# Optimization experiments

Hardware: AMD Instinct MI355X
Metric: run time of the kernel (lower is better)

## Reference

```python
import jax, jax.numpy as jnp
import numpy as np

N_NODES = 150000  # n_users + n_items
N_EDGES = 2400000
D = 128
LEAKY_SLOPE = 0.2  # tf.nn.leaky_relu default alpha
L2_EPS = 1e-12     # tf.math.l2_normalize epsilon


def setup_inputs() -> dict:
    key = jax.random.key(0)
    ks = jax.random.split(key, 8)
    edge_row = jax.random.randint(ks[0], (N_EDGES,), 0, N_NODES, dtype=jnp.int32)
    edge_col = jax.random.randint(ks[1], (N_EDGES,), 0, N_NODES, dtype=jnp.int32)
    edge_val = jax.random.uniform(ks[2], (N_EDGES,), dtype=jnp.float32)
    ego_embeddings = jax.random.normal(ks[3], (N_NODES, D), dtype=jnp.float32)
    w_gc = jax.random.normal(ks[4], (D, D), dtype=jnp.float32) * 0.05
    b_gc = jax.random.normal(ks[5], (D,), dtype=jnp.float32) * 0.05
    w_bi = jax.random.normal(ks[6], (D, D), dtype=jnp.float32) * 0.05
    b_bi = jax.random.normal(ks[7], (D,), dtype=jnp.float32) * 0.05
    return {"edge_row": edge_row, "edge_col": edge_col, "edge_val": edge_val,
            "ego_embeddings": ego_embeddings,
            "w_gc": w_gc, "b_gc": b_gc, "w_bi": w_bi, "b_bi": b_bi}


def reference(edge_row, edge_col, edge_val, ego_embeddings, w_gc, b_gc, w_bi, b_bi):
    # Sparse A @ ego  (concat over n_fold row-blocks == full SpMM)
    msgs = edge_val[:, None] * ego_embeddings[edge_col]          # [E, D]
    side = jax.ops.segment_sum(msgs, edge_row, num_segments=N_NODES)  # [N, D]
    # dual dense transform + leaky_relu
    sum_emb = jax.nn.leaky_relu(side @ w_gc + b_gc, negative_slope=LEAKY_SLOPE)
    bi_emb = jax.nn.leaky_relu((ego_embeddings * side) @ w_bi + b_bi,
                               negative_slope=LEAKY_SLOPE)
    ego = sum_emb + bi_emb
    # dropout rate = 1 - mess_dropout = 0 -> identity (deterministic)
    # tf.math.l2_normalize(axis=1)
    sq = jnp.sum(ego * ego, axis=1, keepdims=True)
    norm_emb = ego * jax.lax.rsqrt(jnp.maximum(sq, L2_EPS))
    return norm_emb
```

## Files before the change

kernel.cpp:

```cpp
#include <hip/hip_runtime.h>
#include <hip/hip_bf16.h>

constexpr int N_NODES = 150000;
constexpr int N_EDGES = 2400000;
constexpr int D       = 128;
constexpr float LEAKY = 0.2f;
constexpr float L2EPS = 1e-12f;

constexpr int NB_SCAN = (N_NODES + 255) / 256;

constexpr int RB_LOG = 9;
constexpr int RB     = 1 << RB_LOG;
constexpr int NBK    = (N_NODES + RB - 1) >> RB_LOG;
constexpr int EPT_A  = 32;
constexpr int EPB_A  = 256 * EPT_A;

typedef short  short8  __attribute__((ext_vector_type(8)));
typedef short  short4v __attribute__((ext_vector_type(4)));
typedef float  f32x4   __attribute__((ext_vector_type(4)));

static __device__ __forceinline__ short f2bf(float x) {
  __hip_bfloat16 h = __float2bfloat16(x);
  return *reinterpret_cast<short*>(&h);
}

__global__ __launch_bounds__(256) void bucket_hist_kernel(
    const int* __restrict__ erow, int* __restrict__ bkt_cnt) {
  __shared__ int h[NBK];
  const int t = threadIdx.x;
  for (int i = t; i < NBK; i += 256) h[i] = 0;
  __syncthreads();
  const long long e0 = (long long)blockIdx.x * EPB_A;
  #pragma unroll
  for (int k = 0; k < EPT_A; ++k) {
    long long e = e0 + k * 256 + t;
    if (e < N_EDGES) atomicAdd(&h[erow[e] >> RB_LOG], 1);
  }
  __syncthreads();
  for (int i = t; i < NBK; i += 256) {
    int c = h[i];
    if (c) atomicAdd(&bkt_cnt[i], c);
  }
}

__global__ __launch_bounds__(512) void bucket_scan_kernel(
    const int* __restrict__ bkt_cnt,
    int* __restrict__ bbase,
    int* __restrict__ bcur,
    int* __restrict__ offs) {
  __shared__ int s[512];
  const int t = threadIdx.x;
  int v = (t < NBK) ? bkt_cnt[t] : 0;
  s[t] = v;
  __syncthreads();
  for (int off = 1; off < 512; off <<= 1) {
    int tmp = (t >= off) ? s[t - off] : 0;
    __syncthreads();
    s[t] += tmp;
    __syncthreads();
  }
  if (t < NBK) {
    int excl = s[t] - v;
    bbase[t] = excl;
    bcur[t]  = excl;
  }
  if (t == 0) { bbase[NBK] = N_EDGES; offs[N_NODES] = N_EDGES; }
}

__global__ __launch_bounds__(256) void hist_kernel(
    const int* __restrict__ erow, int* __restrict__ cnt) {
  int base = blockIdx.x * 2048 + threadIdx.x;
  #pragma unroll
  for (int k = 0; k < 8; ++k) {
    int e = base + k * 256;
    if (e < N_EDGES) atomicAdd(&cnt[erow[e]], 1);
  }
}

__global__ __launch_bounds__(256) void scan_block_sums(
    const int* __restrict__ cnt, int* __restrict__ bsums) {
  __shared__ int s[256];
  int i = blockIdx.x * 256 + threadIdx.x;
  s[threadIdx.x] = (i < N_NODES) ? cnt[i] : 0;
  __syncthreads();
  for (int off = 128; off > 0; off >>= 1) {
    if (threadIdx.x < off) s[threadIdx.x] += s[threadIdx.x + off];
    __syncthreads();
  }
  if (threadIdx.x == 0) bsums[blockIdx.x] = s[0];
}

__global__ __launch_bounds__(1024) void scan_partials(int* __restrict__ bsums) {
  __shared__ int s[1024];
  int v = (threadIdx.x < NB_SCAN) ? bsums[threadIdx.x] : 0;
  s[threadIdx.x] = v;
  __syncthreads();
  for (int off = 1; off < 1024; off <<= 1) {
    int t = (threadIdx.x >= off) ? s[threadIdx.x - off] : 0;
    __syncthreads();
    s[threadIdx.x] += t;
    __syncthreads();
  }
  if (threadIdx.x < NB_SCAN) bsums[threadIdx.x] = s[threadIdx.x] - v;
}

__global__ __launch_bounds__(256) void scan_final(
    const int* __restrict__ cnt, const int* __restrict__ bsums,
    int* __restrict__ offs, int* __restrict__ cursor) {
  __shared__ int s[256];
  int i = blockIdx.x * 256 + threadIdx.x;
  int v = (i < N_NODES) ? cnt[i] : 0;
  s[threadIdx.x] = v;
  __syncthreads();
  for (int off = 1; off < 256; off <<= 1) {
    int t = (threadIdx.x >= off) ? s[threadIdx.x - off] : 0;
    __syncthreads();
    s[threadIdx.x] += t;
    __syncthreads();
  }
  if (i < N_NODES) {
    int excl = s[threadIdx.x] - v + bsums[blockIdx.x];
    offs[i]   = excl;
    cursor[i] = excl;
  }
  if (i == 0) offs[N_NODES] = N_EDGES;
}

__global__ __launch_bounds__(256) void bucket_scatter_kernel(
    const int*   __restrict__ erow,
    const int*   __restrict__ ecol,
    const float* __restrict__ eval,
    int*         __restrict__ bcur,
    int2*        __restrict__ stage) {
  __shared__ int h[NBK];
  __shared__ int basea[NBK];
  const int t = threadIdx.x;
  const long long e0 = (long long)blockIdx.x * EPB_A;

  for (int i = t; i < NBK; i += 256) h[i] = 0;
  __syncthreads();

  int rows[EPT_A];
  #pragma unroll
  for (int k = 0; k < EPT_A; ++k) {
    long long e = e0 + k * 256 + t;
    int r = -1;
    if (e < N_EDGES) { r = erow[e]; atomicAdd(&h[r >> RB_LOG], 1); }
    rows[k] = r;
  }
  __syncthreads();

  for (int b = t; b < NBK; b += 256) {
    int c = h[b];
    basea[b] = c ? atomicAdd(&bcur[b], c) : 0;
    h[b] = 0;
  }
  __syncthreads();

  #pragma unroll
  for (int k = 0; k < EPT_A; ++k) {
    int r = rows[k];
    if (r >= 0) {
      long long e = e0 + k * 256 + t;
      int bkt  = r >> RB_LOG;
      int rank = atomicAdd(&h[bkt], 1);
      int pos  = basea[bkt] + rank;
      int pack = ecol[e] | ((r & (RB - 1)) << 18);
      stage[pos] = make_int2(pack, __float_as_int(eval[e]));
    }
  }
}

__global__ __launch_bounds__(256) void bucket_permute_kernel(
    const int*  __restrict__ bbase,
    const int2* __restrict__ stage,
    int2*       __restrict__ ev,
    int*        __restrict__ offs) {
  __shared__ int cnt[RB];
  __shared__ int s[256];
  const int t    = threadIdx.x;
  const int bkt  = blockIdx.x;
  const int row0 = bkt << RB_LOG;
  const int w0   = bbase[bkt];
  const int w1   = bbase[bkt + 1];

  for (int i = t; i < RB; i += 256) cnt[i] = 0;
  __syncthreads();

  for (int i = w0 + t; i < w1; i += 256) {
    int px = ((const int*)stage)[2 * (size_t)i];
    atomicAdd(&cnt[(px >> 18) & (RB - 1)], 1);
  }
  __syncthreads();

  int c0 = cnt[2 * t], c1 = cnt[2 * t + 1];
  int pairsum = c0 + c1;
  s[t] = pairsum;
  __syncthreads();
  for (int off = 1; off < 256; off <<= 1) {
    int v = (t >= off) ? s[t - off] : 0;
    __syncthreads();
    s[t] += v;
    __syncthreads();
  }
  int pexcl = s[t] - pairsum;
  int e0 = w0 + pexcl;
  int e1 = e0 + c0;
  cnt[2 * t]     = e0;
  cnt[2 * t + 1] = e1;
  int r0 = row0 + 2 * t;
  if (r0 < N_NODES)     offs[r0]     = e0;
  if (r0 + 1 < N_NODES) offs[r0 + 1] = e1;
  __syncthreads();

  for (int i = w0 + t; i < w1; i += 256) {
    int2 e = stage[i];
    int rl  = (e.x >> 18) & (RB - 1);
    int pos = atomicAdd(&cnt[rl], 1);
    ev[pos] = make_int2(e.x & 0x3FFFF, e.y);
  }
}

__global__ __launch_bounds__(256) void bin_kernel(
    const int*   __restrict__ erow,
    const int*   __restrict__ ecol,
    const float* __restrict__ eval,
    int*         __restrict__ cursor,
    int2*        __restrict__ sorted_ev) {
  int base = blockIdx.x * 1024 + threadIdx.x;
  int e0 = base, e1 = base + 256, e2 = base + 512, e3 = base + 768;
  int r0 = (e0 < N_EDGES) ? erow[e0] : 0;
  int r1 = (e1 < N_EDGES) ? erow[e1] : 0;
  int r2 = (e2 < N_EDGES) ? erow[e2] : 0;
  int r3 = (e3 < N_EDGES) ? erow[e3] : 0;
  int p0 = (e0 < N_EDGES) ? atomicAdd(&cursor[r0], 1) : 0;
  int p1 = (e1 < N_EDGES) ? atomicAdd(&cursor[r1], 1) : 0;
  int p2 = (e2 < N_EDGES) ? atomicAdd(&cursor[r2], 1) : 0;
  int p3 = (e3 < N_EDGES) ? atomicAdd(&cursor[r3], 1) : 0;
  if (e0 < N_EDGES) sorted_ev[p0] = make_int2(ecol[e0], __float_as_int(eval[e0]));
  if (e1 < N_EDGES) sorted_ev[p1] = make_int2(ecol[e1], __float_as_int(eval[e1]));
  if (e2 < N_EDGES) sorted_ev[p2] = make_int2(ecol[e2], __float_as_int(eval[e2]));
  if (e3 < N_EDGES) sorted_ev[p3] = make_int2(ecol[e3], __float_as_int(eval[e3]));
}

__global__ __launch_bounds__(256) void conv_ego_kernel(
    const float* __restrict__ ego, short* __restrict__ ebf) {
  int i = blockIdx.x * 256 + threadIdx.x;
  constexpr int TOTAL = N_NODES * D / 4;
  if (i < TOTAL) {
    float4 v = ((const float4*)ego)[i];
    short4v p;
    p[0] = f2bf(v.x); p[1] = f2bf(v.y); p[2] = f2bf(v.z); p[3] = f2bf(v.w);
    ((short4v*)ebf)[i] = p;
  }
}

__global__ __launch_bounds__(128) void prep_weights_kernel(
    const float* __restrict__ wg, const float* __restrict__ wb,
    short* __restrict__ wtg, short* __restrict__ wtb) {
  int n = blockIdx.x;
  int k = threadIdx.x;
  wtg[n * D + k] = f2bf(wg[k * D + n]);
  wtb[n * D + k] = f2bf(wb[k * D + n]);
}

__global__ __launch_bounds__(256) void spmm_bf16_kernel(
    const int*   __restrict__ offs,
    const int2*  __restrict__ ev,
    const short* __restrict__ ebf,
    float*       __restrict__ side) {
  const int t = threadIdx.x;
  const int g = t >> 4;
  const int l = t & 15;
  const int row = blockIdx.x * 16 + g;

  const int s0 = offs[row], s1 = offs[row + 1];
  float a0 = 0.f, a1 = 0.f, a2 = 0.f, a3 = 0.f;
  float a4 = 0.f, a5 = 0.f, a6 = 0.f, a7 = 0.f;

  auto accum = [&](int2 e) {
    uint4 u = *(const uint4*)(ebf + (size_t)e.x * D + l * 8);
    float v = __int_as_float(e.y);
    a0 = fmaf(v, __uint_as_float(u.x << 16), a0);
    a1 = fmaf(v, __uint_as_float(u.x & 0xffff0000u), a1);
    a2 = fmaf(v, __uint_as_float(u.y << 16), a2);
    a3 = fmaf(v, __uint_as_float(u.y & 0xffff0000u), a3);
    a4 = fmaf(v, __uint_as_float(u.z << 16), a4);
    a5 = fmaf(v, __uint_as_float(u.z & 0xffff0000u), a5);
    a6 = fmaf(v, __uint_as_float(u.w << 16), a6);
    a7 = fmaf(v, __uint_as_float(u.w & 0xffff0000u), a7);
  };

  int i = s0;
  const int n4 = s0 + ((s1 - s0) & ~3);
  for (; i < n4; i += 4) {
    int2 e0 = ev[i], e1 = ev[i + 1], e2 = ev[i + 2], e3 = ev[i + 3];
    accum(e0); accum(e1); accum(e2); accum(e3);
  }
  for (; i < s1; ++i) accum(ev[i]);

  float* dst = side + (size_t)row * D + l * 8;
  *(float4*)(dst)     = make_float4(a0, a1, a2, a3);
  *(float4*)(dst + 4) = make_float4(a4, a5, a6, a7);
}

__global__ __launch_bounds__(256) void spmm_kernel(
    const int*  __restrict__ offs,
    const int2* __restrict__ ev,
    const float* __restrict__ ego,
    float*       __restrict__ side) {
  const int t = threadIdx.x;
  const int g = t >> 5;
  const int l = t & 31;
  const int row = blockIdx.x * 8 + g;
  if (row >= N_NODES) return;
  const int s0 = offs[row], s1 = offs[row + 1];
  float ax = 0.f, ay = 0.f, az = 0.f, aw = 0.f;
  int i = s0;
  const int n4 = s0 + ((s1 - s0) & ~3);
  for (; i < n4; i += 4) {
    int2 e0 = ev[i], e1 = ev[i + 1], e2 = ev[i + 2], e3 = ev[i + 3];
    float4 g0 = *(const float4*)(ego + (size_t)e0.x * D + 4 * l);
    float4 g1 = *(const float4*)(ego + (size_t)e1.x * D + 4 * l);
    float4 g2 = *(const float4*)(ego + (size_t)e2.x * D + 4 * l);
    float4 g3 = *(const float4*)(ego + (size_t)e3.x * D + 4 * l);
    float v0 = __int_as_float(e0.y), v1 = __int_as_float(e1.y);
    float v2 = __int_as_float(e2.y), v3 = __int_as_float(e3.y);
    ax = fmaf(v0, g0.x, ax); ay = fmaf(v0, g0.y, ay);
    az = fmaf(v0, g0.z, az); aw = fmaf(v0, g0.w, aw);
    ax = fmaf(v1, g1.x, ax); ay = fmaf(v1, g1.y, ay);
    az = fmaf(v1, g1.z, az); aw = fmaf(v1, g1.w, aw);
    ax = fmaf(v2, g2.x, ax); ay = fmaf(v2, g2.y, ay);
    az = fmaf(v2, g2.z, az); aw = fmaf(v2, g2.w, aw);
    ax = fmaf(v3, g3.x, ax); ay = fmaf(v3, g3.y, ay);
    az = fmaf(v3, g3.z, az); aw = fmaf(v3, g3.w, aw);
  }
  for (; i < s1; ++i) {
    int2 e = ev[i];
    float4 gg = *(const float4*)(ego + (size_t)e.x * D + 4 * l);
    float v = __int_as_float(e.y);
    ax = fmaf(v, gg.x, ax); ay = fmaf(v, gg.y, ay);
    az = fmaf(v, gg.z, az); aw = fmaf(v, gg.w, aw);
  }
  *(float4*)(side + (size_t)row * D + 4 * l) = make_float4(ax, ay, az, aw);
}

__global__ __launch_bounds__(256) void transform_mfma_kernel(
    const float* __restrict__ side,
    const float* __restrict__ ego,
    const short* __restrict__ wtg,
    const short* __restrict__ wtb,
    const float* __restrict__ b_gc,
    const float* __restrict__ b_bi,
    float*       __restrict__ out) {
  __shared__ short sA[16][136];
  __shared__ short sP[16][136];
  __shared__ float sO[16][132];
  __shared__ float sInv[16];

  const int t    = threadIdx.x;
  const int w    = t >> 6;
  const int l    = t & 63;
  const int base = blockIdx.x * 16;

  #pragma unroll
  for (int k = 0; k < 2; ++k) {
    int f  = k * 256 + t;
    int r  = f >> 5;
    int c4 = (f & 31) * 4;
    float4 sv = *(const float4*)(side + (size_t)(base + r) * D + c4);
    float4 ev = *(const float4*)(ego  + (size_t)(base + r) * D + c4);
    short4v pa, pp;
    pa[0] = f2bf(sv.x); pa[1] = f2bf(sv.y); pa[2] = f2bf(sv.z); pa[3] = f2bf(sv.w);
    pp[0] = f2bf(sv.x * ev.x); pp[1] = f2bf(sv.y * ev.y);
    pp[2] = f2bf(sv.z * ev.z); pp[3] = f2bf(sv.w * ev.w);
    *(short4v*)&sA[r][c4] = pa;
    *(short4v*)&sP[r][c4] = pp;
  }
  __syncthreads();

  f32x4 accg[2] = {{0.f, 0.f, 0.f, 0.f}, {0.f, 0.f, 0.f, 0.f}};
  f32x4 accb[2] = {{0.f, 0.f, 0.f, 0.f}, {0.f, 0.f, 0.f, 0.f}};

  const int arow = l & 15;
  const int koff = (l >> 4) * 8;
  const int nb   = w * 32;

  #pragma unroll
  for (int ks = 0; ks < 4; ++ks) {
    const int k0 = ks * 32 + koff;
    short8 a_s = *(const short8*)&sA[arow][k0];
    short8 a_p = *(const short8*)&sP[arow][k0];
    #pragma unroll
    for (int ct = 0; ct < 2; ++ct) {
      const int n = nb + ct * 16 + arow;
      short8 bgf = *(const short8*)(wtg + (size_t)n * D + k0);
      short8 bbf = *(const short8*)(wtb + (size_t)n * D + k0);
      accg[ct] = __builtin_amdgcn_mfma_f32_16x16x32_bf16(a_s, bgf, accg[ct], 0, 0, 0);
      accb[ct] = __builtin_amdgcn_mfma_f32_16x16x32_bf16(a_p, bbf, accb[ct], 0, 0, 0);
    }
  }

  #pragma unroll
  for (int ct = 0; ct < 2; ++ct) {
    const int col = nb + ct * 16 + arow;
    const float bg = b_gc[col];
    const float bb = b_bi[col];
    #pragma unroll
    for (int j = 0; j < 4; ++j) {
      const int r = (l >> 4) * 4 + j;
      float x1 = accg[ct][j] + bg; x1 = (x1 > 0.f) ? x1 : LEAKY * x1;
      float x2 = accb[ct][j] + bb; x2 = (x2 > 0.f) ? x2 : LEAKY * x2;
      sO[r][col] = x1 + x2;
    }
  }
  __syncthreads();

  {
    const int r = t >> 4, c16 = t & 15;
    float sum = 0.f;
    #pragma unroll
    for (int i = 0; i < 8; ++i) {
      float v = sO[r][c16 * 8 + i];
      sum = fmaf(v, v, sum);
    }
    #pragma unroll
    for (int off = 8; off > 0; off >>= 1) sum += __shfl_down(sum, off, 16);
    if (c16 == 0) sInv[r] = rsqrtf(fmaxf(sum, L2EPS));
  }
  __syncthreads();

  #pragma unroll
  for (int k = 0; k < 2; ++k) {
    int f  = k * 256 + t;
    int r  = f >> 5;
    int c4 = (f & 31) * 4;
    float inv = sInv[r];
    float4 v = *(const float4*)&sO[r][c4];
    v.x *= inv; v.y *= inv; v.z *= inv; v.w *= inv;
    *(float4*)(out + (size_t)(base + r) * D + c4) = v;
  }
}

__global__ __launch_bounds__(256) void scatter_kernel(
    const int*   __restrict__ erow,
    const int*   __restrict__ ecol,
    const float* __restrict__ eval,
    const float* __restrict__ ego,
    float*       __restrict__ side) {
  long long t = (long long)blockIdx.x * blockDim.x + threadIdx.x;
  int e = (int)(t >> 5);
  if (e >= N_EDGES) return;
  int c = (int)(t & 31);
  int r  = erow[e];
  int cl = ecol[e];
  float v = eval[e];
  const float4* src = (const float4*)(ego + (long long)cl * D);
  float4 m = src[c];
  float* dst = side + (long long)r * D + c * 4;
  atomicAdd(dst + 0, v * m.x);
  atomicAdd(dst + 1, v * m.y);
  atomicAdd(dst + 2, v * m.z);
  atomicAdd(dst + 3, v * m.w);
}

__global__ __launch_bounds__(128) void transform_f32_kernel(
    const float* __restrict__ side,
    const float* __restrict__ ego,
    const float* __restrict__ w_gc,
    const float* __restrict__ b_gc,
    const float* __restrict__ w_bi,
    const float* __restrict__ b_bi,
    float*       __restrict__ out) {
  constexpr int RPB = 16;
  __shared__ float s_side[RPB][D];
  __shared__ float s_prod[RPB][D];
  __shared__ float s_part[RPB][2];
  const int j    = threadIdx.x;
  const int base = blockIdx.x * RPB;
  #pragma unroll
  for (int r = 0; r < RPB; ++r) {
    int node = base + r;
    float s = 0.f, e = 0.f;
    if (node < N_NODES) {
      s = side[(long long)node * D + j];
      e = ego [(long long)node * D + j];
    }
    s_side[r][j] = s;
    s_prod[r][j] = e * s;
  }
  __syncthreads();
  float acc_gc[RPB], acc_bi[RPB];
  #pragma unroll
  for (int r = 0; r < RPB; ++r) { acc_gc[r] = 0.f; acc_bi[r] = 0.f; }
  for (int k = 0; k < D; ++k) {
    float wg = w_gc[k * D + j];
    float wb = w_bi[k * D + j];
    #pragma unroll
    for (int r = 0; r < RPB; ++r) {
      acc_gc[r] = fmaf(s_side[r][k], wg, acc_gc[r]);
      acc_bi[r] = fmaf(s_prod[r][k], wb, acc_bi[r]);
    }
  }
  const float bg = b_gc[j];
  const float bb = b_bi[j];
  #pragma unroll
  for (int r = 0; r < RPB; ++r) {
    float x1 = acc_gc[r] + bg; x1 = (x1 > 0.f) ? x1 : LEAKY * x1;
    float x2 = acc_bi[r] + bb; x2 = (x2 > 0.f) ? x2 : LEAKY * x2;
    acc_gc[r] = x1 + x2;
  }
  const int lane = j & 63;
  const int wv   = j >> 6;
  #pragma unroll
  for (int r = 0; r < RPB; ++r) {
    float sq = acc_gc[r] * acc_gc[r];
    #pragma unroll
    for (int off = 32; off > 0; off >>= 1) sq += __shfl_down(sq, off, 64);
    if (lane == 0) s_part[r][wv] = sq;
  }
  __syncthreads();
  #pragma unroll
  for (int r = 0; r < RPB; ++r) {
    int node = base + r;
    if (node < N_NODES) {
      float tot = s_part[r][0] + s_part[r][1];
      float inv = rsqrtf(fmaxf(tot, L2EPS));
      out[(long long)node * D + j] = acc_gc[r] * inv;
    }
  }
}

extern "C" void kernel_launch(void* const* d_in, const int* in_sizes, int n_in,
                              void* d_out, int out_size, void* d_ws, size_t ws_size,
                              hipStream_t stream) {
  const int*   erow = (const int*)  d_in[0];
  const int*   ecol = (const int*)  d_in[1];
  const float* eval = (const float*)d_in[2];
  const float* ego  = (const float*)d_in[3];
  const float* w_gc = (const float*)d_in[4];
  const float* b_gc = (const float*)d_in[5];
  const float* w_bi = (const float*)d_in[6];
  const float* b_bi = (const float*)d_in[7];
  float* out = (float*)d_out;

  auto align256 = [](size_t x) { return (x + 255) & ~(size_t)255; };
  size_t off_cnt    = 0;
  size_t off_offs   = align256(off_cnt    + (size_t)N_NODES * 4);
  size_t off_cursor = align256(off_offs   + (size_t)(N_NODES + 1) * 4);
  size_t off_bsums  = align256(off_cursor + (size_t)N_NODES * 4);
  size_t off_bcur   = align256(off_bsums  + 1024 * 4);
  size_t off_wtg    = align256(off_bcur   + (size_t)NBK * 4);
  size_t off_wtb    = align256(off_wtg    + (size_t)D * D * 2);
  size_t off_ev     = align256(off_wtb    + (size_t)D * D * 2);
  size_t off_ebf    = align256(off_ev     + (size_t)N_EDGES * 8);
  size_t ws_mid     = off_ebf;
  size_t ws_sort    = off_ebf + (size_t)N_EDGES * 8;
  size_t ws_full    = off_ebf + (size_t)N_NODES * D * 2;

  if (ws_size >= ws_mid) {
    char* ws = (char*)d_ws;
    int*   cnt    = (int*)  (ws + off_cnt);
    int*   offs   = (int*)  (ws + off_offs);
    int*   cursor = (int*)  (ws + off_cursor);
    int*   bsums  = (int*)  (ws + off_bsums);
    int*   bcur   = (int*)  (ws + off_bcur);
    short* wtg    = (short*)(ws + off_wtg);
    short* wtb    = (short*)(ws + off_wtb);
    int2*  ev     = (int2*) (ws + off_ev);
    short* ebf    = (short*)(ws + off_ebf);
    int2*  stage  = (int2*) (ws + off_ebf);

    float* side = out;

    bool bucketed = (ws_size >= ws_sort);
    if (bucketed) {
      hipMemsetAsync(cnt, 0, (size_t)NBK * 4, stream);
      bucket_hist_kernel<<<(N_EDGES + EPB_A - 1) / EPB_A, 256, 0, stream>>>(erow, cnt);
      bucket_scan_kernel<<<1, 512, 0, stream>>>(cnt, bsums, bcur, offs);
      bucket_scatter_kernel<<<(N_EDGES + EPB_A - 1) / EPB_A, 256, 0, stream>>>(
          erow, ecol, eval, bcur, stage);
      bucket_permute_kernel<<<NBK, 256, 0, stream>>>(bsums, stage, ev, offs);
    } else {
      hipMemsetAsync(cnt, 0, (size_t)N_NODES * 4, stream);
      hist_kernel<<<(N_EDGES + 2047) / 2048, 256, 0, stream>>>(erow, cnt);
      scan_block_sums<<<NB_SCAN, 256, 0, stream>>>(cnt, bsums);
      scan_partials<<<1, 1024, 0, stream>>>(bsums);
      scan_final<<<NB_SCAN, 256, 0, stream>>>(cnt, bsums, offs, cursor);
      bin_kernel<<<(N_EDGES + 1023) / 1024, 256, 0, stream>>>(
          erow, ecol, eval, cursor, ev);
    }
    prep_weights_kernel<<<D, D, 0, stream>>>(w_gc, w_bi, wtg, wtb);

    if (ws_size >= ws_full) {
      conv_ego_kernel<<<(N_NODES * D / 4 + 255) / 256, 256, 0, stream>>>(ego, ebf);
      spmm_bf16_kernel<<<N_NODES / 16, 256, 0, stream>>>(offs, ev, ebf, side);
    } else {
      spmm_kernel<<<(N_NODES + 7) / 8, 256, 0, stream>>>(offs, ev, ego, side);
    }
    transform_mfma_kernel<<<N_NODES / 16, 256, 0, stream>>>(
        side, ego, wtg, wtb, b_gc, b_bi, out);
  } else {
    float* side = out;
    hipMemsetAsync(side, 0, (size_t)N_NODES * D * 4, stream);
    long long total = (long long)N_EDGES * 32;
    int grid = (int)((total + 255) / 256);
    scatter_kernel<<<grid, 256, 0, stream>>>(erow, ecol, eval, ego, side);
    transform_f32_kernel<<<N_NODES / 16, 128, 0, stream>>>(
        side, ego, w_gc, b_gc, w_bi, b_bi, out);
  }
}
```

Before: 438.0 us.

## Fuse bf16 SpMM with MFMA dense transform and L2 normalize epilogue

The bf16 SpMM kernel now feeds each 16-row tile of aggregated embeddings and their product with ego straight into shared memory as bf16. The same block then runs the dual MFMA transform, the leaky ReLU, the bias add and the L2 normalization. This removes the separate transform launch and the fp32 write and re-read of the side matrix through global memory. In exchange, shared memory per block and register pressure go up, which may lower occupancy for the latency-bound gather.

```diff
diff --git a/kernel.cpp b/kernel.cpp
--- a/kernel.cpp
+++ b/kernel.cpp
@@ -264,22 +264,33 @@
   wtb[n * D + k] = f2bf(wb[k * D + n]);
 }
 
-__global__ __launch_bounds__(256) void spmm_bf16_kernel(
+__global__ __launch_bounds__(256) void spmm_transform_kernel(
     const int*   __restrict__ offs,
     const int2*  __restrict__ ev,
     const short* __restrict__ ebf,
-    float*       __restrict__ side) {
-  const int t = threadIdx.x;
-  const int g = t >> 4;
-  const int l = t & 15;
-  const int row = blockIdx.x * 16 + g;
+    const float* __restrict__ ego,
+    const short* __restrict__ wtg,
+    const short* __restrict__ wtb,
+    const float* __restrict__ b_gc,
+    const float* __restrict__ b_bi,
+    float*       __restrict__ out) {
+  __shared__ short sA[16][136];
+  __shared__ short sP[16][136];
+  __shared__ float sO[16][132];
+  __shared__ float sInv[16];
+
+  const int t    = threadIdx.x;
+  const int g    = t >> 4;
+  const int lg   = t & 15;
+  const int base = blockIdx.x * 16;
+  const int row  = base + g;
 
   const int s0 = offs[row], s1 = offs[row + 1];
   float a0 = 0.f, a1 = 0.f, a2 = 0.f, a3 = 0.f;
   float a4 = 0.f, a5 = 0.f, a6 = 0.f, a7 = 0.f;
 
   auto accum = [&](int2 e) {
-    uint4 u = *(const uint4*)(ebf + (size_t)e.x * D + l * 8);
+    uint4 u = *(const uint4*)(ebf + (size_t)e.x * D + lg * 8);
     float v = __int_as_float(e.y);
     a0 = fmaf(v, __uint_as_float(u.x << 16), a0);
     a1 = fmaf(v, __uint_as_float(u.x & 0xffff0000u), a1);
@@ -299,9 +310,89 @@
   }
   for (; i < s1; ++i) accum(ev[i]);
 
-  float* dst = side + (size_t)row * D + l * 8;
-  *(float4*)(dst)     = make_float4(a0, a1, a2, a3);
-  *(float4*)(dst + 4) = make_float4(a4, a5, a6, a7);
+  {
+    const float* er = ego + (size_t)row * D + lg * 8;
+    float4 ev0 = *(const float4*)(er);
+    float4 ev1 = *(const float4*)(er + 4);
+    short4v pa0, pa1, pp0, pp1;
+    pa0[0] = f2bf(a0); pa0[1] = f2bf(a1); pa0[2] = f2bf(a2); pa0[3] = f2bf(a3);
+    pa1[0] = f2bf(a4); pa1[1] = f2bf(a5); pa1[2] = f2bf(a6); pa1[3] = f2bf(a7);
+    pp0[0] = f2bf(a0 * ev0.x); pp0[1] = f2bf(a1 * ev0.y);
+    pp0[2] = f2bf(a2 * ev0.z); pp0[3] = f2bf(a3 * ev0.w);
+    pp1[0] = f2bf(a4 * ev1.x); pp1[1] = f2bf(a5 * ev1.y);
+    pp1[2] = f2bf(a6 * ev1.z); pp1[3] = f2bf(a7 * ev1.w);
+    *(short4v*)&sA[g][lg * 8]     = pa0;
+    *(short4v*)&sA[g][lg * 8 + 4] = pa1;
+    *(short4v*)&sP[g][lg * 8]     = pp0;
+    *(short4v*)&sP[g][lg * 8 + 4] = pp1;
+  }
+  __syncthreads();
+
+  {
+    const int w    = t >> 6;
+    const int l64  = t & 63;
+    const int arow = l64 & 15;
+    const int koff = (l64 >> 4) * 8;
+    const int nb   = w * 32;
+
+    f32x4 accg[2] = {{0.f, 0.f, 0.f, 0.f}, {0.f, 0.f, 0.f, 0.f}};
+    f32x4 accb[2] = {{0.f, 0.f, 0.f, 0.f}, {0.f, 0.f, 0.f, 0.f}};
+
+    #pragma unroll
+    for (int ks = 0; ks < 4; ++ks) {
+      const int k0 = ks * 32 + koff;
+      short8 a_s = *(const short8*)&sA[arow][k0];
+      short8 a_p = *(const short8*)&sP[arow][k0];
+      #pragma unroll
+      for (int ct = 0; ct < 2; ++ct) {
+        const int n = nb + ct * 16 + arow;
+        short8 bgf = *(const short8*)(wtg + (size_t)n * D + k0);
+        short8 bbf = *(const short8*)(wtb + (size_t)n * D + k0);
+        accg[ct] = __builtin_amdgcn_mfma_f32_16x16x32_bf16(a_s, bgf, accg[ct], 0, 0, 0);
+        accb[ct] = __builtin_amdgcn_mfma_f32_16x16x32_bf16(a_p, bbf, accb[ct], 0, 0, 0);
+      }
+    }
+
+    #pragma unroll
+    for (int ct = 0; ct < 2; ++ct) {
+      const int col = nb + ct * 16 + arow;
+      const float bg = b_gc[col];
+      const float bb = b_bi[col];
+      #pragma unroll
+      for (int j = 0; j < 4; ++j) {
+        const int r = (l64 >> 4) * 4 + j;
+        float x1 = accg[ct][j] + bg; x1 = (x1 > 0.f) ? x1 : LEAKY * x1;
+        float x2 = accb[ct][j] + bb; x2 = (x2 > 0.f) ? x2 : LEAKY * x2;
+        sO[r][col] = x1 + x2;
+      }
+    }
+  }
+  __syncthreads();
+
+  {
+    const int r = t >> 4, c16 = t & 15;
+    float sum = 0.f;
+    #pragma unroll
+    for (int i2 = 0; i2 < 8; ++i2) {
+      float v = sO[r][c16 * 8 + i2];
+      sum = fmaf(v, v, sum);
+    }
+    #pragma unroll
+    for (int off = 8; off > 0; off >>= 1) sum += __shfl_down(sum, off, 16);
+    if (c16 == 0) sInv[r] = rsqrtf(fmaxf(sum, L2EPS));
+  }
+  __syncthreads();
+
+  #pragma unroll
+  for (int k = 0; k < 2; ++k) {
+    int f  = k * 256 + t;
+    int r  = f >> 5;
+    int c4 = (f & 31) * 4;
+    float inv = sInv[r];
+    float4 v = *(const float4*)&sO[r][c4];
+    v.x *= inv; v.y *= inv; v.z *= inv; v.w *= inv;
+    *(float4*)(out + (size_t)(base + r) * D + c4) = v;
+  }
 }
 
 __global__ __launch_bounds__(256) void spmm_kernel(
@@ -571,8 +662,6 @@
     short* ebf    = (short*)(ws + off_ebf);
     int2*  stage  = (int2*) (ws + off_ebf);
 
-    float* side = out;
-
     bool bucketed = (ws_size >= ws_sort);
     if (bucketed) {
       hipMemsetAsync(cnt, 0, (size_t)NBK * 4, stream);
@@ -594,12 +683,14 @@
 
     if (ws_size >= ws_full) {
       conv_ego_kernel<<<(N_NODES * D / 4 + 255) / 256, 256, 0, stream>>>(ego, ebf);
-      spmm_bf16_kernel<<<N_NODES / 16, 256, 0, stream>>>(offs, ev, ebf, side);
+      spmm_transform_kernel<<<N_NODES / 16, 256, 0, stream>>>(
+          offs, ev, ebf, ego, wtg, wtb, b_gc, b_bi, out);
     } else {
+      float* side = out;
       spmm_kernel<<<(N_NODES + 7) / 8, 256, 0, stream>>>(offs, ev, ego, side);
-    }
-    transform_mfma_kernel<<<N_NODES / 16, 256, 0, stream>>>(
-        side, ego, wtg, wtb, b_gc, b_bi, out);
+      transform_mfma_kernel<<<N_NODES / 16, 256, 0, stream>>>(
+          side, ego, wtg, wtb, b_gc, b_bi, out);
+    }
   } else {
     float* side = out;
     hipMemsetAsync(side, 0, (size_t)N_NODES * D * 4, stream);
```

New measurement: 409.8 us. 1.07x faster.
